# Kernel tuning notes

Hardware: AMD Instinct MI355X
Metric: run time of the kernel (lower is better)

The kernel has to match this reference:

```python
import jax, jax.numpy as jnp
import numpy as np

B = 2048
L = 32000  # num_labels
E = 4      # number of experts


def setup_inputs() -> dict:
    key = jax.random.key(0)
    ks = jax.random.split(key, 5)
    labels = jax.random.randint(ks[0], (B,), 0, L)
    logits = [jax.random.normal(ks[i + 1], (B, L), dtype=jnp.float32) for i in range(E)]
    return {
        "labels": labels,
        "logits0": logits[0],
        "logits1": logits[1],
        "logits2": logits[2],
        "logits3": logits[3],
    }


def reference(labels, logits0, logits1, logits2, logits3):
    # stacked: (B, L, E)
    stacked = jnp.stack([logits0, logits1, logits2, logits3], axis=2)
    # per-expert predictions: (B, E)
    predictions = jnp.argmax(stacked, axis=1)
    correct = predictions == labels[:, None]  # (B, E) bool
    any_correct = jnp.any(correct, axis=1)  # (B,)
    # first correct expert index (argmax of bool returns first True)
    first_correct = jnp.argmax(correct, axis=1)  # (B,)
    # logits at the true label for each expert: (B, E)
    label_logits = jnp.take_along_axis(stacked, labels[:, None, None], axis=1)[:, 0, :]
    conf_best = jnp.argmax(label_logits, axis=1)  # (B,)
    best_expert = jnp.where(any_correct, first_correct, conf_best)  # (B,)
    # gather the chosen expert's logits: (B, L)
    effective = jnp.take_along_axis(stacked, best_expert[:, None, None], axis=2)[:, :, 0]
    return effective
```

## Files before the change

### kernel.cpp

```cpp
#include <hip/hip_runtime.h>

#define ROW_L 32000
#define NT    256
#define NV    (ROW_L / 4)
#define UF    8

typedef float f32x4 __attribute__((ext_vector_type(4)));

__global__ __launch_bounds__(NT) void oracle_best_expert_kernel(
    const int* __restrict__ labels,
    const float* __restrict__ g0,
    const float* __restrict__ g1,
    const float* __restrict__ g2,
    const float* __restrict__ g3,
    float* __restrict__ out)
{
    const int b = blockIdx.x;
    const size_t row = (size_t)b * ROW_L;
    const float* __restrict__ p0 = g0 + row;
    const float* __restrict__ p1 = g1 + row;
    const float* __restrict__ p2 = g2 + row;
    const float* __restrict__ p3 = g3 + row;

    const int tid  = threadIdx.x;
    const int wave = tid >> 6;
    const int lane = tid & 63;

    __shared__ float s_labv[4];
    __shared__ float s_max[4];
    __shared__ int   s_idx[4];
    __shared__ int   s_best;

    const float* __restrict__ pw = (wave == 0) ? p0 :
                                   (wave == 1) ? p1 :
                                   (wave == 2) ? p2 : p3;
    const f32x4* __restrict__ q = (const f32x4*)pw;

    const int lab = labels[b];
    if (lane == 0) s_labv[wave] = pw[lab];

    float m  = -__builtin_inff();
    int   mi = 0;

#pragma unroll 1
    for (int it = 0; it < 15; ++it) {
        const int base = it * (UF * 64) + lane;
        f32x4 v[UF];
#pragma unroll
        for (int u = 0; u < UF; ++u) v[u] = q[base + u * 64];
#pragma unroll
        for (int u = 0; u < UF; ++u) {
            const int bi = (base + u * 64) * 4;
            if (v[u].x > m) { m = v[u].x; mi = bi + 0; }
            if (v[u].y > m) { m = v[u].y; mi = bi + 1; }
            if (v[u].z > m) { m = v[u].z; mi = bi + 2; }
            if (v[u].w > m) { m = v[u].w; mi = bi + 3; }
        }
    }
    {
        const int base = 15 * (UF * 64) + lane;
        f32x4 v[5];
#pragma unroll
        for (int u = 0; u < 5; ++u) v[u] = q[base + u * 64];
#pragma unroll
        for (int u = 0; u < 5; ++u) {
            const int bi = (base + u * 64) * 4;
            if (v[u].x > m) { m = v[u].x; mi = bi + 0; }
            if (v[u].y > m) { m = v[u].y; mi = bi + 1; }
            if (v[u].z > m) { m = v[u].z; mi = bi + 2; }
            if (v[u].w > m) { m = v[u].w; mi = bi + 3; }
        }
    }

#pragma unroll
    for (int off = 32; off >= 1; off >>= 1) {
        const float ov = __shfl_down(m, off, 64);
        const int   oi = __shfl_down(mi, off, 64);
        if (ov > m || (ov == m && oi < mi)) { m = ov; mi = oi; }
    }
    if (lane == 0) { s_max[wave] = m; s_idx[wave] = mi; }
    __syncthreads();

    if (tid == 0) {
        int best = -1;
#pragma unroll
        for (int e = 0; e < 4; ++e)
            if (best < 0 && s_idx[e] == lab) best = e;
        if (best < 0) {
            float bm = s_labv[0]; best = 0;
#pragma unroll
            for (int e = 1; e < 4; ++e)
                if (s_labv[e] > bm) { bm = s_labv[e]; best = e; }
        }
        s_best = best;
    }
    __syncthreads();

    const int be = s_best;
    const f32x4* __restrict__ src = (const f32x4*)((be == 0) ? p0 :
                                                   (be == 1) ? p1 :
                                                   (be == 2) ? p2 : p3);
    f32x4* __restrict__ dst = (f32x4*)(out + row);
#pragma unroll 1
    for (int i0 = tid; i0 < NV; i0 += NT * UF) {
        f32x4 t[UF];
#pragma unroll
        for (int u = 0; u < UF; ++u) {
            const int i = i0 + u * NT;
            if (i < NV) t[u] = src[i];
        }
#pragma unroll
        for (int u = 0; u < UF; ++u) {
            const int i = i0 + u * NT;
            if (i < NV) __builtin_nontemporal_store(t[u], &dst[i]);
        }
    }
}

extern "C" void kernel_launch(void* const* d_in, const int* in_sizes, int n_in,
                              void* d_out, int out_size, void* d_ws, size_t ws_size,
                              hipStream_t stream) {
    const int*   labels = (const int*)d_in[0];
    const float* g0     = (const float*)d_in[1];
    const float* g1     = (const float*)d_in[2];
    const float* g2     = (const float*)d_in[3];
    const float* g3     = (const float*)d_in[4];
    float*       out    = (float*)d_out;

    const int B = in_sizes[0];
    oracle_best_expert_kernel<<<B, NT, 0, stream>>>(labels, g0, g1, g2, g3, out);
}
```

Before: 267.7 us.

## Speculatively write confidence-best expert row during argmax scan with double-buffered loads

```diff
diff --git a/kernel.cpp b/kernel.cpp
--- a/kernel.cpp
+++ b/kernel.cpp
@@ -6,6 +6,27 @@
 #define UF    8
 
 typedef float f32x4 __attribute__((ext_vector_type(4)));
+
+#define LOADB(dst, kk) do {                                                  \
+    const int base_ = (kk) * (UF * 64) + lane;                               \
+    _Pragma("unroll")                                                        \
+    for (int u = 0; u < UF; ++u) dst[u] = q[base_ + u * 64];                 \
+    __builtin_amdgcn_sched_barrier(0);                                       \
+} while (0)
+
+#define CONSUME(src, kk) do {                                                \
+    const int base_ = (kk) * (UF * 64) + lane;                               \
+    _Pragma("unroll")                                                        \
+    for (int u = 0; u < UF; ++u) {                                           \
+        const f32x4 v = src[u];                                              \
+        const int bi = (base_ + u * 64) * 4;                                 \
+        if (v.x > m) { m = v.x; mi = bi + 0; }                               \
+        if (v.y > m) { m = v.y; mi = bi + 1; }                               \
+        if (v.z > m) { m = v.z; mi = bi + 2; }                               \
+        if (v.w > m) { m = v.w; mi = bi + 3; }                               \
+        if (do_store) __builtin_nontemporal_store(v, &qo[base_ + u * 64]);   \
+    }                                                                        \
+} while (0)
 
 __global__ __launch_bounds__(NT) void oracle_best_expert_kernel(
     const int* __restrict__ labels,
@@ -29,46 +50,51 @@
     __shared__ float s_labv[4];
     __shared__ float s_max[4];
     __shared__ int   s_idx[4];
-    __shared__ int   s_best;
+    __shared__ int   s_fix;
 
     const float* __restrict__ pw = (wave == 0) ? p0 :
                                    (wave == 1) ? p1 :
                                    (wave == 2) ? p2 : p3;
-    const f32x4* __restrict__ q = (const f32x4*)pw;
+    const f32x4* __restrict__ q  = (const f32x4*)pw;
+    f32x4* __restrict__       qo = (f32x4*)(out + row);
 
     const int lab = labels[b];
     if (lane == 0) s_labv[wave] = pw[lab];
+    __syncthreads();
+    const float c0 = s_labv[0], c1 = s_labv[1], c2 = s_labv[2], c3 = s_labv[3];
+    int cb = 0; float bm = c0;
+    if (c1 > bm) { bm = c1; cb = 1; }
+    if (c2 > bm) { bm = c2; cb = 2; }
+    if (c3 > bm) { bm = c3; cb = 3; }
+    const bool do_store = (wave == cb);
 
     float m  = -__builtin_inff();
     int   mi = 0;
 
+    f32x4 Abuf[UF], Bbuf[UF];
+    LOADB(Abuf, 0);
 #pragma unroll 1
-    for (int it = 0; it < 15; ++it) {
-        const int base = it * (UF * 64) + lane;
-        f32x4 v[UF];
+    for (int k = 0; k < 14; k += 2) {
+        LOADB(Bbuf, k + 1);
+        CONSUME(Abuf, k);
+        LOADB(Abuf, k + 2);
+        CONSUME(Bbuf, k + 1);
+    }
+    CONSUME(Abuf, 14);
+    {
+        const int base_ = 15 * (UF * 64) + lane;
+        f32x4 T[5];
 #pragma unroll
-        for (int u = 0; u < UF; ++u) v[u] = q[base + u * 64];
-#pragma unroll
-        for (int u = 0; u < UF; ++u) {
-            const int bi = (base + u * 64) * 4;
-            if (v[u].x > m) { m = v[u].x; mi = bi + 0; }
-            if (v[u].y > m) { m = v[u].y; mi = bi + 1; }
-            if (v[u].z > m) { m = v[u].z; mi = bi + 2; }
-            if (v[u].w > m) { m = v[u].w; mi = bi + 3; }
-        }
-    }
-    {
-        const int base = 15 * (UF * 64) + lane;
-        f32x4 v[5];
-#pragma unroll
-        for (int u = 0; u < 5; ++u) v[u] = q[base + u * 64];
+        for (int u = 0; u < 5; ++u) T[u] = q[base_ + u * 64];
 #pragma unroll
         for (int u = 0; u < 5; ++u) {
-            const int bi = (base + u * 64) * 4;
-            if (v[u].x > m) { m = v[u].x; mi = bi + 0; }
-            if (v[u].y > m) { m = v[u].y; mi = bi + 1; }
-            if (v[u].z > m) { m = v[u].z; mi = bi + 2; }
-            if (v[u].w > m) { m = v[u].w; mi = bi + 3; }
+            const f32x4 v = T[u];
+            const int bi = (base_ + u * 64) * 4;
+            if (v.x > m) { m = v.x; mi = bi + 0; }
+            if (v.y > m) { m = v.y; mi = bi + 1; }
+            if (v.z > m) { m = v.z; mi = bi + 2; }
+            if (v.w > m) { m = v.w; mi = bi + 3; }
+            if (do_store) __builtin_nontemporal_store(v, &qo[base_ + u * 64]);
         }
     }
 
@@ -86,34 +112,18 @@
 #pragma unroll
         for (int e = 0; e < 4; ++e)
             if (best < 0 && s_idx[e] == lab) best = e;
-        if (best < 0) {
-            float bm = s_labv[0]; best = 0;
-#pragma unroll
-            for (int e = 1; e < 4; ++e)
-                if (s_labv[e] > bm) { bm = s_labv[e]; best = e; }
-        }
-        s_best = best;
+        if (best < 0) best = cb;
+        s_fix = (best == cb) ? -1 : best;
     }
     __syncthreads();
 
-    const int be = s_best;
-    const f32x4* __restrict__ src = (const f32x4*)((be == 0) ? p0 :
-                                                   (be == 1) ? p1 :
-                                                   (be == 2) ? p2 : p3);
-    f32x4* __restrict__ dst = (f32x4*)(out + row);
-#pragma unroll 1
-    for (int i0 = tid; i0 < NV; i0 += NT * UF) {
-        f32x4 t[UF];
-#pragma unroll
-        for (int u = 0; u < UF; ++u) {
-            const int i = i0 + u * NT;
-            if (i < NV) t[u] = src[i];
-        }
-#pragma unroll
-        for (int u = 0; u < UF; ++u) {
-            const int i = i0 + u * NT;
-            if (i < NV) __builtin_nontemporal_store(t[u], &dst[i]);
-        }
+    const int fx = s_fix;
+    if (fx >= 0) {
+        const f32x4* __restrict__ src = (const f32x4*)((fx == 0) ? p0 :
+                                                       (fx == 1) ? p1 :
+                                                       (fx == 2) ? p2 : p3);
+        for (int i = tid; i < NV; i += NT)
+            __builtin_nontemporal_store(src[i], &qo[i]);
     }
 }
 
```

After: 272.8 us. About the same (+1.9%).
